# Kernel optimization log

Measured on AMD Instinct MI355X. Metric: run time of the kernel, lower is better.

The kernel has to match this reference:

```python
import jax, jax.numpy as jnp
import numpy as np

N, C, H, W = 32, 512, 56, 56
L, CT, HEAD, GROUPS = 64, 512, 16, 16
SIZE, POS_DIM = 14, 49  # PosEncoder(size=14, num_downsample=1) -> 14^2 // 4 = 49


def setup_inputs() -> dict:
    key = jax.random.key(0)
    ks = jax.random.split(key, 8)
    return {
        "feature": jax.random.normal(ks[0], (N, C, H, W), jnp.float32),
        "w_tc": jax.random.normal(ks[1], (L, C), jnp.float32) * 0.02,
        "b_tc": jnp.zeros((L,), jnp.float32),
        "w_val": jax.random.normal(ks[2], (GROUPS, CT // GROUPS, C // GROUPS), jnp.float32) * 0.02,
        "b_val": jnp.zeros((CT,), jnp.float32),
        "w_ds3": jax.random.normal(ks[3], (1, 1, 3, 3), jnp.float32) * 0.1,
        "b_ds3": jnp.zeros((1,), jnp.float32),
        "w_ds1": jax.random.normal(ks[4], (1, 1), jnp.float32) * 0.1,
        "b_ds1": jnp.zeros((1,), jnp.float32),
        "w_pos": jax.random.normal(ks[5], (POS_DIM, POS_DIM), jnp.float32) * 0.02,
        "b_pos": jnp.zeros((POS_DIM,), jnp.float32),
        "w_tok": jax.random.normal(ks[6], (CT, CT + POS_DIM), jnp.float32) * 0.02,
        "b_tok": jnp.zeros((CT,), jnp.float32),
    }


def reference(feature, w_tc, b_tc, w_val, b_val, w_ds3, b_ds3, w_ds1, b_ds1,
              w_pos, b_pos, w_tok, b_tok):
    n, c, h, w = feature.shape
    hw = h * w
    # --- static token coefficients: 1x1 conv C->L, scale, softmax over HW ---
    tc = jnp.einsum('nchw,lc->nlhw', feature, w_tc) + b_tc[None, :, None, None]
    tc = tc.reshape(n, 1, L, hw).transpose(0, 1, 3, 2) / np.sqrt(c)  # (N,1,HW,L)
    tc = jax.nn.softmax(tc, axis=2)
    # --- grouped 1x1 conv value: C -> CT (groups=16) ---
    fg = feature.reshape(n, GROUPS, c // GROUPS, hw)
    val = jnp.einsum('ngci,gdc->ngdi', fg, w_val).reshape(n, CT, hw) + b_val[None, :, None]
    val = val.reshape(n, HEAD, CT // HEAD, hw)
    # --- token aggregation: (N,h,CT/h,HW) @ (N,1,HW,L) -> (N,CT,L) ---
    tokens = jnp.matmul(val, tc).reshape(n, CT, -1)
    # --- PosEncoder: view coef maps as images, nearest-resize to 14x14 ---
    pc = tc.reshape(n * L, 1, h, w)  # torch .view memory reinterpretation
    ih = (jnp.arange(SIZE) * h) // SIZE
    iw = (jnp.arange(SIZE) * w) // SIZE
    pc = pc[:, :, ih][:, :, :, iw]  # (N*L,1,14,14) nearest interpolate
    # conv3x3 stride 2 pad 1: 14 -> 7
    pc = jax.lax.conv_general_dilated(pc, w_ds3, (2, 2), ((1, 1), (1, 1))) + b_ds3[None, :, None, None]
    # conv1x1 (1->1)
    pc = jnp.einsum('nchw,dc->ndhw', pc, w_ds1) + b_ds1[None, :, None, None]
    pc = pc.reshape(n, L, POS_DIM).transpose(0, 2, 1)  # (N,49,L)
    pos = jnp.einsum('ncl,dc->ndl', pc, w_pos) + b_pos[None, :, None]
    # --- concat + final 1x1 conv1d (CT+49 -> CT) ---
    tokens = jnp.concatenate([tokens, pos], axis=1)
    tokens = jnp.einsum('ncl,dc->ndl', tokens, w_tok) + b_tok[None, :, None]
    return tokens  # (N, CT, L)
```

## Files before the change

kernel.cpp:

```cpp
#include <hip/hip_runtime.h>
#include <cstddef>
#include <cstdint>

namespace {

constexpr int kN = 32;
constexpr int kC = 512;
constexpr int kHW = 3136;
constexpr int kL = 64;
constexpr int kCT = 512;
constexpr int kTok = 561;
constexpr int kKcat = 576;

typedef float fx4 __attribute__((ext_vector_type(4)));
typedef float f32x4 __attribute__((ext_vector_type(4)));
typedef short short8 __attribute__((ext_vector_type(8)));
typedef unsigned int u32x2 __attribute__((ext_vector_type(2)));

static __device__ inline unsigned pack_bf16(float a, float b) {
  unsigned ua = __builtin_bit_cast(unsigned, a) + 0x8000u;
  unsigned ub = __builtin_bit_cast(unsigned, b) + 0x8000u;
  return __builtin_amdgcn_perm(ub, ua, 0x07060302u);
}

__global__ __launch_bounds__(256) void build_wcat_kernel(
    const float* __restrict__ w_tok, const float* __restrict__ w_val,
    float* __restrict__ wcat) {
  int idx = blockIdx.x * 256 + threadIdx.x;
  if (idx >= kCT * kKcat) return;
  int d = idx / kKcat;
  int c = idx - d * kKcat;
  float v = 0.f;
  if (c < kCT) {
    int g = c >> 5, k = c & 31;
    const float* wt = w_tok + (size_t)d * kTok + g * 32;
    const float* wv = w_val + g * 1024 + k;
    float s = 0.f;
#pragma unroll
    for (int dp = 0; dp < 32; ++dp) s += wt[dp] * wv[dp * 32];
    v = s;
  } else if (c < kTok) {
    v = w_tok[(size_t)d * kTok + c];
  }
  wcat[idx] = v;
}

__global__ __launch_bounds__(256) void build_cst_kernel(
    const float* __restrict__ w_tok, const float* __restrict__ b_val,
    const float* __restrict__ b_tok, float* __restrict__ cst) {
  int d = blockIdx.x * 256 + threadIdx.x;
  if (d >= kCT) return;
  float s = b_tok[d];
  for (int c = 0; c < kCT; ++c) s += w_tok[(size_t)d * kTok + c] * b_val[c];
  cst[d] = s;
}

__global__ __launch_bounds__(256) void zero_pad_kernel(float* __restrict__ bcat) {
  int i = blockIdx.x * 256 + threadIdx.x;
  const int tot = kN * kL * (kKcat - kTok);
  if (i >= tot) return;
  int n = i / (kL * 15);
  int r = i - n * (kL * 15);
  int l = r / 15;
  int k = kTok + (r - l * 15);
  bcat[(size_t)n * kL * kKcat + (size_t)l * kKcat + k] = 0.f;
}

__global__ __launch_bounds__(256) void tc_gemm_kernel(
    const float* __restrict__ feat, const float* __restrict__ w_tc,
    const float* __restrict__ b_tc, float* __restrict__ tcT) {
  const int n = blockIdx.y;
  const int pb = blockIdx.x * 256;
  const int tid = threadIdx.x;
  const int wave = tid >> 6, lane = tid & 63;
  const int quad = lane >> 4, l16 = lane & 15;
  __shared__ unsigned short As[64][72];
  __shared__ unsigned short Bs[256][72];
  __shared__ float bsm[64];
  if (tid < 64) bsm[tid] = b_tc[tid];

  f32x4 acc[4][4];
#pragma unroll
  for (int i = 0; i < 4; ++i)
#pragma unroll
    for (int j = 0; j < 4; ++j) acc[i][j] = (f32x4){0.f, 0.f, 0.f, 0.f};

  const float* fb = feat + (size_t)n * kC * kHW;
  const int al = tid & 63, akg = (tid >> 6) * 16;
  const int bc4 = (tid & 15) * 4, bpl0 = (tid >> 4) * 4;

  for (int c0 = 0; c0 < kC; c0 += 64) {
    const float* asrc = w_tc + (size_t)al * kC + c0 + akg;
#pragma unroll
    for (int u = 0; u < 4; ++u) {
      fx4 v = *(const fx4*)(asrc + u * 4);
      u32x2 w = {pack_bf16(v[0], v[1]), pack_bf16(v[2], v[3])};
      *(u32x2*)&As[al][akg + u * 4] = w;
    }
#pragma unroll
    for (int pass = 0; pass < 4; ++pass) {
      int pl = bpl0 + pass * 64;
      int pe = pb + pl;
      pe = pe < 3132 ? pe : 3132;
      fx4 v0 = *(const fx4*)(fb + (size_t)(c0 + bc4 + 0) * kHW + pe);
      fx4 v1 = *(const fx4*)(fb + (size_t)(c0 + bc4 + 1) * kHW + pe);
      fx4 v2 = *(const fx4*)(fb + (size_t)(c0 + bc4 + 2) * kHW + pe);
      fx4 v3 = *(const fx4*)(fb + (size_t)(c0 + bc4 + 3) * kHW + pe);
#pragma unroll
      for (int j = 0; j < 4; ++j) {
        u32x2 w = {pack_bf16(v0[j], v1[j]), pack_bf16(v2[j], v3[j])};
        *(u32x2*)&Bs[pl + j][bc4] = w;
      }
    }
    __syncthreads();
#pragma unroll
    for (int ks = 0; ks < 2; ++ks) {
      short8 a[4], b[4];
#pragma unroll
      for (int i = 0; i < 4; ++i)
        a[i] = *(const short8*)&As[i * 16 + l16][ks * 32 + quad * 8];
#pragma unroll
      for (int j = 0; j < 4; ++j)
        b[j] = *(const short8*)&Bs[wave * 64 + j * 16 + l16][ks * 32 + quad * 8];
#pragma unroll
      for (int i = 0; i < 4; ++i)
#pragma unroll
        for (int j = 0; j < 4; ++j)
          acc[i][j] = __builtin_amdgcn_mfma_f32_16x16x32_bf16(a[i], b[j], acc[i][j], 0, 0, 0);
    }
    __syncthreads();
  }

  const float inv = 0.04419417382415922f;
  float* ob = tcT + (size_t)n * kL * kHW;
#pragma unroll
  for (int ti = 0; ti < 4; ++ti) {
#pragma unroll
    for (int tj = 0; tj < 4; ++tj) {
      int pg = pb + wave * 64 + tj * 16 + l16;
      if (pg < kHW) {
#pragma unroll
        for (int r = 0; r < 4; ++r) {
          int l = ti * 16 + quad * 4 + r;
          ob[(size_t)l * kHW + pg] = (acc[ti][tj][r] + bsm[l]) * inv;
        }
      }
    }
  }
}

__global__ __launch_bounds__(256) void softmax_stats_kernel(
    const float* __restrict__ tcT, float* __restrict__ mArr,
    float* __restrict__ invArr) {
  const int row = blockIdx.x * 4 + (threadIdx.x >> 6);
  const int lane = threadIdx.x & 63;
  const float* src = tcT + (size_t)row * kHW + lane * 4;
  fx4 x[13];
#pragma unroll
  for (int i = 0; i < 12; ++i) x[i] = *(const fx4*)(src + i * 256);
  if (lane < 16)
    x[12] = *(const fx4*)(src + 3072);
  else
    x[12] = (fx4){-1e30f, -1e30f, -1e30f, -1e30f};
  float m = -1e30f;
#pragma unroll
  for (int i = 0; i < 13; ++i)
    m = fmaxf(m, fmaxf(fmaxf(x[i][0], x[i][1]), fmaxf(x[i][2], x[i][3])));
#pragma unroll
  for (int off = 32; off >= 1; off >>= 1) m = fmaxf(m, __shfl_xor(m, off));
  float s = 0.f;
#pragma unroll
  for (int i = 0; i < 13; ++i) {
    s += __expf(x[i][0] - m) + __expf(x[i][1] - m) + __expf(x[i][2] - m) +
         __expf(x[i][3] - m);
  }
#pragma unroll
  for (int off = 32; off >= 1; off >>= 1) s += __shfl_xor(s, off);
  if (lane == 0) {
    mArr[row] = m;
    invArr[row] = 1.f / s;
  }
}

__global__ __launch_bounds__(256) void m_gemm_kernel(
    const float* __restrict__ feat, const float* __restrict__ tcT,
    const float* __restrict__ mArr, const float* __restrict__ invArr,
    float* __restrict__ part, int klen) {
  const int cb = blockIdx.x * 256;
  const int n = blockIdx.y;
  const int s = blockIdx.z;
  const int p0s = s * klen;
  const int tid = threadIdx.x;
  const int wave = tid >> 6, lane = tid & 63;
  const int quad = lane >> 4, l16 = lane & 15;
  __shared__ unsigned short As[64][72];
  __shared__ unsigned short Bs[256][72];

  const int al = tid & 63, akg = (tid >> 6) * 16;
  const float sm = mArr[n * 64 + al];
  const float si = invArr[n * 64 + al];

  f32x4 acc[4][4];
#pragma unroll
  for (int i = 0; i < 4; ++i)
#pragma unroll
    for (int j = 0; j < 4; ++j) acc[i][j] = (f32x4){0.f, 0.f, 0.f, 0.f};

  const float* tb = tcT + (size_t)(n * 64 + al) * kHW;
  const float* fb = feat + (size_t)n * kC * kHW;
  const int bkg = (tid >> 6) * 16, bcr = tid & 63;

  for (int p0 = p0s; p0 < p0s + klen; p0 += 64) {
#pragma unroll
    for (int u = 0; u < 4; ++u) {
      fx4 v = *(const fx4*)(tb + p0 + akg + u * 4);
      float e0 = __expf(v[0] - sm) * si;
      float e1 = __expf(v[1] - sm) * si;
      float e2 = __expf(v[2] - sm) * si;
      float e3 = __expf(v[3] - sm) * si;
      u32x2 w = {pack_bf16(e0, e1), pack_bf16(e2, e3)};
      *(u32x2*)&As[al][akg + u * 4] = w;
    }
#pragma unroll
    for (int pass = 0; pass < 4; ++pass) {
      int c = cb + pass * 64 + bcr;
      const float* src = fb + (size_t)c * kHW + p0 + bkg;
#pragma unroll
      for (int u = 0; u < 4; ++u) {
        fx4 v = *(const fx4*)(src + u * 4);
        u32x2 w = {pack_bf16(v[0], v[1]), pack_bf16(v[2], v[3])};
        *(u32x2*)&Bs[pass * 64 + bcr][bkg + u * 4] = w;
      }
    }
    __syncthreads();
#pragma unroll
    for (int ks = 0; ks < 2; ++ks) {
      short8 a[4], b[4];
#pragma unroll
      for (int i = 0; i < 4; ++i)
        a[i] = *(const short8*)&As[i * 16 + l16][ks * 32 + quad * 8];
#pragma unroll
      for (int j = 0; j < 4; ++j)
        b[j] = *(const short8*)&Bs[wave * 64 + j * 16 + l16][ks * 32 + quad * 8];
#pragma unroll
      for (int i = 0; i < 4; ++i)
#pragma unroll
        for (int j = 0; j < 4; ++j)
          acc[i][j] = __builtin_amdgcn_mfma_f32_16x16x32_bf16(a[i], b[j], acc[i][j], 0, 0, 0);
    }
    __syncthreads();
  }

  float* ob = part + (size_t)(s * kN + n) * kL * kCT;
#pragma unroll
  for (int ti = 0; ti < 4; ++ti) {
#pragma unroll
    for (int tj = 0; tj < 4; ++tj) {
      int cg = cb + wave * 64 + tj * 16 + l16;
#pragma unroll
      for (int r = 0; r < 4; ++r) {
        int l = ti * 16 + quad * 4 + r;
        ob[(size_t)l * kCT + cg] = acc[ti][tj][r];
      }
    }
  }
}

__global__ __launch_bounds__(256) void reduce_m_kernel(
    const float* __restrict__ part, float* __restrict__ bcat, int ksplit) {
  int i = blockIdx.x * 256 + threadIdx.x;
  if (i >= kN * kL * kCT) return;
  int n = i >> 15;
  int r = i & 32767;
  int l = r >> 9;
  int c = r & 511;
  float s = 0.f;
  for (int ss = 0; ss < ksplit; ++ss)
    s += part[(size_t)ss * kN * kL * kCT + i];
  bcat[(size_t)n * kL * kKcat + (size_t)l * kKcat + c] = s;
}

__global__ __launch_bounds__(256) void pos_conv_kernel(
    const float* __restrict__ tcT, const float* __restrict__ mArr,
    const float* __restrict__ invArr, const float* __restrict__ w3,
    const float* __restrict__ b3, const float* __restrict__ w1,
    const float* __restrict__ b1, float* __restrict__ pcl) {
  int idx = blockIdx.x * 256 + threadIdx.x;
  if (idx >= kN * kL * 49) return;
  int n = idx / (kL * 49);
  int r = idx - n * (kL * 49);
  int lp = r / 49;
  int o = r - lp * 49;
  int y = o / 7, x = o - y * 7;
  const float* tb = tcT + (size_t)n * kL * kHW;
  const float* mB = mArr + n * 64;
  const float* iB = invArr + n * 64;
  float a = 0.f;
#pragma unroll
  for (int dy = 0; dy < 3; ++dy) {
    int i = 2 * y - 1 + dy;
    if (i < 0 || i >= 14) continue;
#pragma unroll
    for (int dx = 0; dx < 3; ++dx) {
      int j = 2 * x - 1 + dx;
      if (j < 0 || j >= 14) continue;
      int t = 224 * i + 4 * j;
      int lsm = t & 63;
      int p = lp * 49 + (t >> 6);
      float raw = tb[(size_t)lsm * kHW + p];
      a += w3[dy * 3 + dx] * (__expf(raw - mB[lsm]) * iB[lsm]);
    }
  }
  pcl[idx] = (a + b3[0]) * w1[0] + b1[0];
}

__global__ __launch_bounds__(256) void pos_out_kernel(
    const float* __restrict__ pcl, const float* __restrict__ wp,
    const float* __restrict__ bp, float* __restrict__ bcat) {
  const int n = blockIdx.x;
  __shared__ float t[64 * 49];
  for (int i = threadIdx.x; i < 64 * 49; i += 256)
    t[i] = pcl[(size_t)n * 64 * 49 + i];
  __syncthreads();
  for (int o = threadIdx.x; o < 64 * 49; o += 256) {
    int l = o / 49, d = o - l * 49;
    float s = bp[d];
#pragma unroll 7
    for (int q = 0; q < 49; ++q) s += wp[d * 49 + q] * t[l * 49 + q];
    bcat[(size_t)n * kL * kKcat + (size_t)l * kKcat + kCT + d] = s;
  }
}

__global__ __launch_bounds__(256) void out_gemm_kernel(
    const float* __restrict__ wcat, const float* __restrict__ bcat,
    const float* __restrict__ cst, float* __restrict__ out) {
  const int db = blockIdx.x * 128;
  const int n = blockIdx.y;
  const int tid = threadIdx.x;
  const int wave = tid >> 6, lane = tid & 63;
  const int quad = lane >> 4, l16 = lane & 15;
  __shared__ unsigned short As[128][72];
  __shared__ unsigned short Bs[64][72];
  __shared__ float csm[128];
  if (tid < 128) csm[tid] = cst[db + tid];

  f32x4 acc[2][4];
#pragma unroll
  for (int i = 0; i < 2; ++i)
#pragma unroll
    for (int j = 0; j < 4; ++j) acc[i][j] = (f32x4){0.f, 0.f, 0.f, 0.f};

  const int ad = tid & 127, akg = (tid >> 7) * 32;
  const int bl = tid & 63, bkg = (tid >> 6) * 16;
  const float* ab = wcat + (size_t)(db + ad) * kKcat + akg;
  const float* bb = bcat + (size_t)n * kL * kKcat + (size_t)bl * kKcat + bkg;

  for (int k0 = 0; k0 < kKcat; k0 += 64) {
#pragma unroll
    for (int u = 0; u < 8; ++u) {
      fx4 v = *(const fx4*)(ab + k0 + u * 4);
      u32x2 w = {pack_bf16(v[0], v[1]), pack_bf16(v[2], v[3])};
      *(u32x2*)&As[ad][akg + u * 4] = w;
    }
#pragma unroll
    for (int u = 0; u < 4; ++u) {
      fx4 v = *(const fx4*)(bb + k0 + u * 4);
      u32x2 w = {pack_bf16(v[0], v[1]), pack_bf16(v[2], v[3])};
      *(u32x2*)&Bs[bl][bkg + u * 4] = w;
    }
    __syncthreads();
#pragma unroll
    for (int ks = 0; ks < 2; ++ks) {
      short8 a[2], b[4];
#pragma unroll
      for (int i = 0; i < 2; ++i)
        a[i] = *(const short8*)&As[wave * 32 + i * 16 + l16][ks * 32 + quad * 8];
#pragma unroll
      for (int j = 0; j < 4; ++j)
        b[j] = *(const short8*)&Bs[j * 16 + l16][ks * 32 + quad * 8];
#pragma unroll
      for (int i = 0; i < 2; ++i)
#pragma unroll
        for (int j = 0; j < 4; ++j)
          acc[i][j] = __builtin_amdgcn_mfma_f32_16x16x32_bf16(a[i], b[j], acc[i][j], 0, 0, 0);
    }
    __syncthreads();
  }

  float* ob = out + (size_t)n * kCT * kL;
#pragma unroll
  for (int ti = 0; ti < 2; ++ti) {
#pragma unroll
    for (int tj = 0; tj < 4; ++tj) {
      int lg = tj * 16 + l16;
#pragma unroll
      for (int r = 0; r < 4; ++r) {
        int dl = wave * 32 + ti * 16 + quad * 4 + r;
        ob[(size_t)(db + dl) * kL + lg] = acc[ti][tj][r] + csm[dl];
      }
    }
  }
}

}

extern "C" void kernel_launch(void* const* d_in, const int* in_sizes, int n_in,
                              void* d_out, int out_size, void* d_ws,
                              size_t ws_size, hipStream_t stream) {
  (void)in_sizes; (void)n_in; (void)out_size;
  const float* feat  = (const float*)d_in[0];
  const float* w_tc  = (const float*)d_in[1];
  const float* b_tc  = (const float*)d_in[2];
  const float* w_val = (const float*)d_in[3];
  const float* b_val = (const float*)d_in[4];
  const float* w_ds3 = (const float*)d_in[5];
  const float* b_ds3 = (const float*)d_in[6];
  const float* w_ds1 = (const float*)d_in[7];
  const float* b_ds1 = (const float*)d_in[8];
  const float* w_pos = (const float*)d_in[9];
  const float* b_pos = (const float*)d_in[10];
  const float* w_tok = (const float*)d_in[11];
  const float* b_tok = (const float*)d_in[12];
  float* out = (float*)d_out;

  float* ws = (float*)d_ws;
  size_t off = 0;
  float* tcT = ws + off;    off += (size_t)kN * kL * kHW;
  float* bcat = ws + off;   off += (size_t)kN * kL * kKcat;
  float* wcat = ws + off;   off += (size_t)kCT * kKcat;
  float* cst = ws + off;    off += kCT;
  float* mArr = ws + off;   off += kN * 64;
  float* invArr = ws + off; off += kN * 64;
  float* pcl = ws + off;    off += (size_t)kN * kL * 49;
  int ksplit = 7;
  if (ws_size < (off + (size_t)7 * kN * kL * kCT) * sizeof(float)) ksplit = 1;
  float* part = ws + off;

  build_wcat_kernel<<<(kCT * kKcat + 255) / 256, 256, 0, stream>>>(w_tok, w_val, wcat);
  build_cst_kernel<<<2, 256, 0, stream>>>(w_tok, b_val, b_tok, cst);
  zero_pad_kernel<<<(kN * kL * 15 + 255) / 256, 256, 0, stream>>>(bcat);
  tc_gemm_kernel<<<dim3(13, kN), 256, 0, stream>>>(feat, w_tc, b_tc, tcT);
  softmax_stats_kernel<<<kN * kL / 4, 256, 0, stream>>>(tcT, mArr, invArr);
  m_gemm_kernel<<<dim3(2, kN, ksplit), 256, 0, stream>>>(
      feat, tcT, mArr, invArr, part, kHW / ksplit);
  reduce_m_kernel<<<(kN * kL * kCT + 255) / 256, 256, 0, stream>>>(part, bcat, ksplit);
  pos_conv_kernel<<<(kN * kL * 49 + 255) / 256, 256, 0, stream>>>(
      tcT, mArr, invArr, w_ds3, b_ds3, w_ds1, b_ds1, pcl);
  pos_out_kernel<<<kN, 256, 0, stream>>>(pcl, w_pos, b_pos, bcat);
  out_gemm_kernel<<<dim3(4, kN), 256, 0, stream>>>(wcat, bcat, cst, out);
}
```

Before: 447.3 us.

## Fuse softmax exp into tc GEMM, store bf16 intermediates, prefetch-pipeline GEMMs

The prep kernels are merged into one launch that also converts w_tc to bf16 and zeroes the denominators. The tc GEMM now applies exp directly and writes unnormalized bf16 exponentials. It accumulates per-row sums with shared and global atomics, so the separate softmax-stats pass and the max subtraction go away. The feature GEMMs use register double-buffered global loads and read the A operand straight from global bf16. Reduce and pos-conv are fused, and the output GEMM reads bf16 operands directly without LDS staging. Skipping the max subtraction risks overflow for large logits, and bf16 intermediates reduce precision.

Result: faster. 436.1 us (-2.5%).

```diff
diff --git a/kernel.cpp b/kernel.cpp
--- a/kernel.cpp
+++ b/kernel.cpp
@@ -1,4 +1,5 @@
 #include <hip/hip_runtime.h>
+#include <hip/hip_bf16.h>
 #include <cstddef>
 #include <cstdint>
 
@@ -17,67 +18,93 @@
 typedef short short8 __attribute__((ext_vector_type(8)));
 typedef unsigned int u32x2 __attribute__((ext_vector_type(2)));
 
-static __device__ inline unsigned pack_bf16(float a, float b) {
-  unsigned ua = __builtin_bit_cast(unsigned, a) + 0x8000u;
-  unsigned ub = __builtin_bit_cast(unsigned, b) + 0x8000u;
-  return __builtin_amdgcn_perm(ub, ua, 0x07060302u);
-}
-
-__global__ __launch_bounds__(256) void build_wcat_kernel(
+static __device__ inline unsigned short bf16_1(float x) {
+  __hip_bfloat16 h = __float2bfloat16(x);
+  unsigned short u;
+  __builtin_memcpy(&u, &h, 2);
+  return u;
+}
+static __device__ inline unsigned pk2(float a, float b) {
+  __hip_bfloat162 h2 = __float22bfloat162_rn(make_float2(a, b));
+  unsigned u;
+  __builtin_memcpy(&u, &h2, 4);
+  return u;
+}
+static __device__ inline float bf2f(unsigned short h) {
+  unsigned u = (unsigned)h << 16;
+  float f;
+  __builtin_memcpy(&f, &u, 4);
+  return f;
+}
+
+__global__ __launch_bounds__(256) void prep_kernel(
     const float* __restrict__ w_tok, const float* __restrict__ w_val,
-    float* __restrict__ wcat) {
+    const float* __restrict__ b_val, const float* __restrict__ b_tok,
+    const float* __restrict__ w_tc, unsigned short* __restrict__ wcat16,
+    float* __restrict__ cst, unsigned short* __restrict__ wtc16,
+    float* __restrict__ denom, unsigned short* __restrict__ bcat16) {
   int idx = blockIdx.x * 256 + threadIdx.x;
-  if (idx >= kCT * kKcat) return;
-  int d = idx / kKcat;
-  int c = idx - d * kKcat;
-  float v = 0.f;
-  if (c < kCT) {
-    int g = c >> 5, k = c & 31;
-    const float* wt = w_tok + (size_t)d * kTok + g * 32;
-    const float* wv = w_val + g * 1024 + k;
-    float s = 0.f;
-#pragma unroll
-    for (int dp = 0; dp < 32; ++dp) s += wt[dp] * wv[dp * 32];
-    v = s;
-  } else if (c < kTok) {
-    v = w_tok[(size_t)d * kTok + c];
-  }
-  wcat[idx] = v;
-}
-
-__global__ __launch_bounds__(256) void build_cst_kernel(
-    const float* __restrict__ w_tok, const float* __restrict__ b_val,
-    const float* __restrict__ b_tok, float* __restrict__ cst) {
-  int d = blockIdx.x * 256 + threadIdx.x;
-  if (d >= kCT) return;
-  float s = b_tok[d];
-  for (int c = 0; c < kCT; ++c) s += w_tok[(size_t)d * kTok + c] * b_val[c];
-  cst[d] = s;
-}
-
-__global__ __launch_bounds__(256) void zero_pad_kernel(float* __restrict__ bcat) {
-  int i = blockIdx.x * 256 + threadIdx.x;
-  const int tot = kN * kL * (kKcat - kTok);
-  if (i >= tot) return;
-  int n = i / (kL * 15);
-  int r = i - n * (kL * 15);
-  int l = r / 15;
-  int k = kTok + (r - l * 15);
-  bcat[(size_t)n * kL * kKcat + (size_t)l * kKcat + k] = 0.f;
-}
-
-__global__ __launch_bounds__(256) void tc_gemm_kernel(
-    const float* __restrict__ feat, const float* __restrict__ w_tc,
-    const float* __restrict__ b_tc, float* __restrict__ tcT) {
+  if (idx < kCT * kKcat) {
+    int d = idx / kKcat;
+    int c = idx - d * kKcat;
+    float v = 0.f;
+    if (c < kCT) {
+      int g = c >> 5, k = c & 31;
+      const float* wt = w_tok + (size_t)d * kTok + g * 32;
+      const float* wv = w_val + g * 1024 + k;
+      float s = 0.f;
+#pragma unroll
+      for (int dp = 0; dp < 32; ++dp) s += wt[dp] * wv[dp * 32];
+      v = s;
+    } else if (c < kTok) {
+      v = w_tok[(size_t)d * kTok + c];
+    }
+    wcat16[idx] = bf16_1(v);
+    return;
+  }
+  idx -= kCT * kKcat;
+  if (idx < kCT) {
+    float s = b_tok[idx];
+    for (int c = 0; c < kCT; ++c) s += w_tok[(size_t)idx * kTok + c] * b_val[c];
+    cst[idx] = s;
+    return;
+  }
+  idx -= kCT;
+  if (idx < kL * kC) {
+    wtc16[idx] = bf16_1(w_tc[idx]);
+    return;
+  }
+  idx -= kL * kC;
+  if (idx < kN * kL) {
+    denom[idx] = 0.f;
+    return;
+  }
+  idx -= kN * kL;
+  if (idx < kN * kL * 15) {
+    int n = idx / (kL * 15);
+    int r = idx - n * (kL * 15);
+    int l = r / 15;
+    int k = kTok + (r - l * 15);
+    bcat16[(size_t)n * kL * kKcat + (size_t)l * kKcat + k] = 0;
+  }
+}
+
+__global__ __launch_bounds__(256) void tc_gemm2_kernel(
+    const float* __restrict__ feat, const unsigned short* __restrict__ wtc16,
+    const float* __restrict__ b_tc, unsigned short* __restrict__ expT,
+    float* __restrict__ denom) {
   const int n = blockIdx.y;
   const int pb = blockIdx.x * 256;
   const int tid = threadIdx.x;
   const int wave = tid >> 6, lane = tid & 63;
   const int quad = lane >> 4, l16 = lane & 15;
-  __shared__ unsigned short As[64][72];
   __shared__ unsigned short Bs[256][72];
   __shared__ float bsm[64];
-  if (tid < 64) bsm[tid] = b_tc[tid];
+  __shared__ float denom_s[64];
+  if (tid < 64) {
+    bsm[tid] = b_tc[tid];
+    denom_s[tid] = 0.f;
+  }
 
   f32x4 acc[4][4];
 #pragma unroll
@@ -86,39 +113,45 @@
     for (int j = 0; j < 4; ++j) acc[i][j] = (f32x4){0.f, 0.f, 0.f, 0.f};
 
   const float* fb = feat + (size_t)n * kC * kHW;
-  const int al = tid & 63, akg = (tid >> 6) * 16;
   const int bc4 = (tid & 15) * 4, bpl0 = (tid >> 4) * 4;
-
-  for (int c0 = 0; c0 < kC; c0 += 64) {
-    const float* asrc = w_tc + (size_t)al * kC + c0 + akg;
-#pragma unroll
-    for (int u = 0; u < 4; ++u) {
-      fx4 v = *(const fx4*)(asrc + u * 4);
-      u32x2 w = {pack_bf16(v[0], v[1]), pack_bf16(v[2], v[3])};
-      *(u32x2*)&As[al][akg + u * 4] = w;
-    }
+  int pe_[4];
+#pragma unroll
+  for (int pass = 0; pass < 4; ++pass) {
+    int pe = pb + bpl0 + pass * 64;
+    pe_[pass] = pe < 3132 ? pe : 3132;
+  }
+
+  fx4 va[4][4], vb[4][4];
+  auto LOADT = [&](int c0, fx4 (&v)[4][4]) {
 #pragma unroll
     for (int pass = 0; pass < 4; ++pass) {
-      int pl = bpl0 + pass * 64;
-      int pe = pb + pl;
-      pe = pe < 3132 ? pe : 3132;
-      fx4 v0 = *(const fx4*)(fb + (size_t)(c0 + bc4 + 0) * kHW + pe);
-      fx4 v1 = *(const fx4*)(fb + (size_t)(c0 + bc4 + 1) * kHW + pe);
-      fx4 v2 = *(const fx4*)(fb + (size_t)(c0 + bc4 + 2) * kHW + pe);
-      fx4 v3 = *(const fx4*)(fb + (size_t)(c0 + bc4 + 3) * kHW + pe);
+      const float* s = fb + (size_t)(c0 + bc4) * kHW + pe_[pass];
+#pragma unroll
+      for (int r = 0; r < 4; ++r) v[pass][r] = *(const fx4*)(s + (size_t)r * kHW);
+    }
+  };
+  auto STORET = [&](fx4 (&v)[4][4]) {
+#pragma unroll
+    for (int pass = 0; pass < 4; ++pass) {
+      int pl = bpl0 + pass * 4 * 16;
+      (void)pl;
+      int base = bpl0 + pass * 64;
 #pragma unroll
       for (int j = 0; j < 4; ++j) {
-        u32x2 w = {pack_bf16(v0[j], v1[j]), pack_bf16(v2[j], v3[j])};
-        *(u32x2*)&Bs[pl + j][bc4] = w;
+        u32x2 w = {pk2(v[pass][0][j], v[pass][1][j]),
+                   pk2(v[pass][2][j], v[pass][3][j])};
+        *(u32x2*)&Bs[base + j][bc4] = w;
       }
     }
-    __syncthreads();
+  };
+  auto COMPUTE = [&](int c0) {
 #pragma unroll
     for (int ks = 0; ks < 2; ++ks) {
       short8 a[4], b[4];
 #pragma unroll
       for (int i = 0; i < 4; ++i)
-        a[i] = *(const short8*)&As[i * 16 + l16][ks * 32 + quad * 8];
+        a[i] = *(const short8*)(wtc16 + (size_t)(i * 16 + l16) * kC + c0 +
+                                ks * 32 + quad * 8);
 #pragma unroll
       for (int j = 0; j < 4; ++j)
         b[j] = *(const short8*)&Bs[wave * 64 + j * 16 + l16][ks * 32 + quad * 8];
@@ -126,65 +159,74 @@
       for (int i = 0; i < 4; ++i)
 #pragma unroll
         for (int j = 0; j < 4; ++j)
-          acc[i][j] = __builtin_amdgcn_mfma_f32_16x16x32_bf16(a[i], b[j], acc[i][j], 0, 0, 0);
-    }
+          acc[i][j] = __builtin_amdgcn_mfma_f32_16x16x32_bf16(a[i], b[j],
+                                                              acc[i][j], 0, 0, 0);
+    }
+  };
+
+  LOADT(0, va);
+#pragma unroll
+  for (int c0 = 0; c0 < kC; c0 += 128) {
+    STORET(va);
+    __syncthreads();
+    LOADT(c0 + 64, vb);
+    COMPUTE(c0);
+    __syncthreads();
+    STORET(vb);
+    __syncthreads();
+    if (c0 + 128 < kC) LOADT(c0 + 128, va);
+    COMPUTE(c0 + 64);
     __syncthreads();
   }
 
   const float inv = 0.04419417382415922f;
-  float* ob = tcT + (size_t)n * kL * kHW;
+  unsigned short* eb = expT + (size_t)n * kL * kHW;
+  float dsum[4][4];
+#pragma unroll
+  for (int ti = 0; ti < 4; ++ti)
+#pragma unroll
+    for (int r = 0; r < 4; ++r) dsum[ti][r] = 0.f;
+
 #pragma unroll
   for (int ti = 0; ti < 4; ++ti) {
 #pragma unroll
     for (int tj = 0; tj < 4; ++tj) {
       int pg = pb + wave * 64 + tj * 16 + l16;
-      if (pg < kHW) {
-#pragma unroll
-        for (int r = 0; r < 4; ++r) {
-          int l = ti * 16 + quad * 4 + r;
-          ob[(size_t)l * kHW + pg] = (acc[ti][tj][r] + bsm[l]) * inv;
+      bool ok = pg < kHW;
+#pragma unroll
+      for (int r = 0; r < 4; ++r) {
+        int l = ti * 16 + quad * 4 + r;
+        float e = 0.f;
+        if (ok) {
+          float raw = (acc[ti][tj][r] + bsm[l]) * inv;
+          unsigned short h = bf16_1(__expf(raw));
+          eb[(size_t)l * kHW + pg] = h;
+          e = bf2f(h);
         }
+        dsum[ti][r] += e;
       }
     }
   }
-}
-
-__global__ __launch_bounds__(256) void softmax_stats_kernel(
-    const float* __restrict__ tcT, float* __restrict__ mArr,
-    float* __restrict__ invArr) {
-  const int row = blockIdx.x * 4 + (threadIdx.x >> 6);
-  const int lane = threadIdx.x & 63;
-  const float* src = tcT + (size_t)row * kHW + lane * 4;
-  fx4 x[13];
-#pragma unroll
-  for (int i = 0; i < 12; ++i) x[i] = *(const fx4*)(src + i * 256);
-  if (lane < 16)
-    x[12] = *(const fx4*)(src + 3072);
-  else
-    x[12] = (fx4){-1e30f, -1e30f, -1e30f, -1e30f};
-  float m = -1e30f;
-#pragma unroll
-  for (int i = 0; i < 13; ++i)
-    m = fmaxf(m, fmaxf(fmaxf(x[i][0], x[i][1]), fmaxf(x[i][2], x[i][3])));
-#pragma unroll
-  for (int off = 32; off >= 1; off >>= 1) m = fmaxf(m, __shfl_xor(m, off));
-  float s = 0.f;
-#pragma unroll
-  for (int i = 0; i < 13; ++i) {
-    s += __expf(x[i][0] - m) + __expf(x[i][1] - m) + __expf(x[i][2] - m) +
-         __expf(x[i][3] - m);
-  }
-#pragma unroll
-  for (int off = 32; off >= 1; off >>= 1) s += __shfl_xor(s, off);
-  if (lane == 0) {
-    mArr[row] = m;
-    invArr[row] = 1.f / s;
-  }
-}
-
-__global__ __launch_bounds__(256) void m_gemm_kernel(
-    const float* __restrict__ feat, const float* __restrict__ tcT,
-    const float* __restrict__ mArr, const float* __restrict__ invArr,
+#pragma unroll
+  for (int off = 1; off < 16; off <<= 1) {
+#pragma unroll
+    for (int ti = 0; ti < 4; ++ti)
+#pragma unroll
+      for (int r = 0; r < 4; ++r) dsum[ti][r] += __shfl_xor(dsum[ti][r], off);
+  }
+  if (l16 == 0) {
+#pragma unroll
+    for (int ti = 0; ti < 4; ++ti)
+#pragma unroll
+      for (int r = 0; r < 4; ++r)
+        atomicAdd(&denom_s[ti * 16 + quad * 4 + r], dsum[ti][r]);
+  }
+  __syncthreads();
+  if (tid < 64) atomicAdd(&denom[n * 64 + tid], denom_s[tid]);
+}
+
+__global__ __launch_bounds__(256) void m_gemm2_kernel(
+    const float* __restrict__ feat, const unsigned short* __restrict__ expT,
     float* __restrict__ part, int klen) {
   const int cb = blockIdx.x * 256;
   const int n = blockIdx.y;
@@ -193,52 +235,46 @@
   const int tid = threadIdx.x;
   const int wave = tid >> 6, lane = tid & 63;
   const int quad = lane >> 4, l16 = lane & 15;
-  __shared__ unsigned short As[64][72];
   __shared__ unsigned short Bs[256][72];
 
-  const int al = tid & 63, akg = (tid >> 6) * 16;
-  const float sm = mArr[n * 64 + al];
-  const float si = invArr[n * 64 + al];
-
   f32x4 acc[4][4];
 #pragma unroll
   for (int i = 0; i < 4; ++i)
 #pragma unroll
     for (int j = 0; j < 4; ++j) acc[i][j] = (f32x4){0.f, 0.f, 0.f, 0.f};
 
-  const float* tb = tcT + (size_t)(n * 64 + al) * kHW;
   const float* fb = feat + (size_t)n * kC * kHW;
+  const unsigned short* ebase = expT + (size_t)n * kL * kHW;
   const int bkg = (tid >> 6) * 16, bcr = tid & 63;
 
-  for (int p0 = p0s; p0 < p0s + klen; p0 += 64) {
-#pragma unroll
-    for (int u = 0; u < 4; ++u) {
-      fx4 v = *(const fx4*)(tb + p0 + akg + u * 4);
-      float e0 = __expf(v[0] - sm) * si;
-      float e1 = __expf(v[1] - sm) * si;
-      float e2 = __expf(v[2] - sm) * si;
-      float e3 = __expf(v[3] - sm) * si;
-      u32x2 w = {pack_bf16(e0, e1), pack_bf16(e2, e3)};
-      *(u32x2*)&As[al][akg + u * 4] = w;
-    }
+  fx4 va[4][4], vb[4][4];
+  auto LOADT = [&](int p0, fx4 (&v)[4][4]) {
 #pragma unroll
     for (int pass = 0; pass < 4; ++pass) {
-      int c = cb + pass * 64 + bcr;
-      const float* src = fb + (size_t)c * kHW + p0 + bkg;
+      const float* src = fb + (size_t)(cb + pass * 64 + bcr) * kHW + p0 + bkg;
+#pragma unroll
+      for (int u = 0; u < 4; ++u) v[pass][u] = *(const fx4*)(src + u * 4);
+    }
+  };
+  auto STORET = [&](fx4 (&v)[4][4]) {
+#pragma unroll
+    for (int pass = 0; pass < 4; ++pass) {
 #pragma unroll
       for (int u = 0; u < 4; ++u) {
-        fx4 v = *(const fx4*)(src + u * 4);
-        u32x2 w = {pack_bf16(v[0], v[1]), pack_bf16(v[2], v[3])};
+        u32x2 w = {pk2(v[pass][u][0], v[pass][u][1]),
+                   pk2(v[pass][u][2], v[pass][u][3])};
         *(u32x2*)&Bs[pass * 64 + bcr][bkg + u * 4] = w;
       }
     }
-    __syncthreads();
+  };
+  auto COMPUTE = [&](int p0) {
 #pragma unroll
     for (int ks = 0; ks < 2; ++ks) {
       short8 a[4], b[4];
 #pragma unroll
       for (int i = 0; i < 4; ++i)
-        a[i] = *(const short8*)&As[i * 16 + l16][ks * 32 + quad * 8];
+        a[i] = *(const short8*)(ebase + (size_t)(i * 16 + l16) * kHW + p0 +
+                                ks * 32 + quad * 8);
 #pragma unroll
       for (int j = 0; j < 4; ++j)
         b[j] = *(const short8*)&Bs[wave * 64 + j * 16 + l16][ks * 32 + quad * 8];
@@ -246,9 +282,28 @@
       for (int i = 0; i < 4; ++i)
 #pragma unroll
         for (int j = 0; j < 4; ++j)
-          acc[i][j] = __builtin_amdgcn_mfma_f32_16x16x32_bf16(a[i], b[j], acc[i][j], 0, 0, 0);
-    }
-    __syncthreads();
+          acc[i][j] = __builtin_amdgcn_mfma_f32_16x16x32_bf16(a[i], b[j],
+                                                              acc[i][j], 0, 0, 0);
+    }
+  };
+
+  const int nk = klen >> 6;
+  LOADT(p0s, va);
+  for (int t = 0; t < nk; t += 2) {
+    const int p0 = p0s + t * 64;
+    STORET(va);
+    __syncthreads();
+    const bool more1 = (t + 1) < nk;
+    if (more1) LOADT(p0 + 64, vb);
+    COMPUTE(p0);
+    __syncthreads();
+    if (more1) {
+      STORET(vb);
+      __syncthreads();
+      if (t + 2 < nk) LOADT(p0 + 128, va);
+      COMPUTE(p0 + 64);
+      __syncthreads();
+    }
   }
 
   float* ob = part + (size_t)(s * kN + n) * kL * kCT;
@@ -266,35 +321,34 @@
   }
 }
 
-__global__ __launch_bounds__(256) void reduce_m_kernel(
-    const float* __restrict__ part, float* __restrict__ bcat, int ksplit) {
-  int i = blockIdx.x * 256 + threadIdx.x;
-  if (i >= kN * kL * kCT) return;
-  int n = i >> 15;
-  int r = i & 32767;
-  int l = r >> 9;
-  int c = r & 511;
-  float s = 0.f;
-  for (int ss = 0; ss < ksplit; ++ss)
-    s += part[(size_t)ss * kN * kL * kCT + i];
-  bcat[(size_t)n * kL * kKcat + (size_t)l * kKcat + c] = s;
-}
-
-__global__ __launch_bounds__(256) void pos_conv_kernel(
-    const float* __restrict__ tcT, const float* __restrict__ mArr,
-    const float* __restrict__ invArr, const float* __restrict__ w3,
-    const float* __restrict__ b3, const float* __restrict__ w1,
-    const float* __restrict__ b1, float* __restrict__ pcl) {
+__global__ __launch_bounds__(256) void reduce_pos_kernel(
+    const float* __restrict__ part, const float* __restrict__ denom,
+    unsigned short* __restrict__ bcat16, const unsigned short* __restrict__ expT,
+    const float* __restrict__ w3, const float* __restrict__ b3,
+    const float* __restrict__ w1, const float* __restrict__ b1,
+    float* __restrict__ pcl, int ksplit) {
   int idx = blockIdx.x * 256 + threadIdx.x;
+  if (idx < kN * kL * kCT) {
+    int n = idx >> 15;
+    int r = idx & 32767;
+    int l = r >> 9;
+    int c = r & 511;
+    float s = 0.f;
+    for (int ss = 0; ss < ksplit; ++ss)
+      s += part[(size_t)ss * (kN * kL * kCT) + idx];
+    float si = 1.f / denom[n * 64 + l];
+    bcat16[(size_t)n * kL * kKcat + (size_t)l * kKcat + c] = bf16_1(s * si);
+    return;
+  }
+  idx -= kN * kL * kCT;
   if (idx >= kN * kL * 49) return;
   int n = idx / (kL * 49);
   int r = idx - n * (kL * 49);
   int lp = r / 49;
   int o = r - lp * 49;
   int y = o / 7, x = o - y * 7;
-  const float* tb = tcT + (size_t)n * kL * kHW;
-  const float* mB = mArr + n * 64;
-  const float* iB = invArr + n * 64;
+  const unsigned short* eb = expT + (size_t)n * kL * kHW;
+  const float* dB = denom + n * 64;
   float a = 0.f;
 #pragma unroll
   for (int dy = 0; dy < 3; ++dy) {
@@ -307,16 +361,16 @@
       int t = 224 * i + 4 * j;
       int lsm = t & 63;
       int p = lp * 49 + (t >> 6);
-      float raw = tb[(size_t)lsm * kHW + p];
-      a += w3[dy * 3 + dx] * (__expf(raw - mB[lsm]) * iB[lsm]);
-    }
-  }
-  pcl[idx] = (a + b3[0]) * w1[0] + b1[0];
-}
-
-__global__ __launch_bounds__(256) void pos_out_kernel(
+      float e = bf2f(eb[(size_t)lsm * kHW + p]);
+      a += w3[dy * 3 + dx] * (e / dB[lsm]);
+    }
+  }
+  pcl[(size_t)n * kL * 49 + lp * 49 + o] = (a + b3[0]) * w1[0] + b1[0];
+}
+
+__global__ __launch_bounds__(256) void pos_out2_kernel(
     const float* __restrict__ pcl, const float* __restrict__ wp,
-    const float* __restrict__ bp, float* __restrict__ bcat) {
+    const float* __restrict__ bp, unsigned short* __restrict__ bcat16) {
   const int n = blockIdx.x;
   __shared__ float t[64 * 49];
   for (int i = threadIdx.x; i < 64 * 49; i += 256)
@@ -327,77 +381,49 @@
     float s = bp[d];
 #pragma unroll 7
     for (int q = 0; q < 49; ++q) s += wp[d * 49 + q] * t[l * 49 + q];
-    bcat[(size_t)n * kL * kKcat + (size_t)l * kKcat + kCT + d] = s;
-  }
-}
-
-__global__ __launch_bounds__(256) void out_gemm_kernel(
-    const float* __restrict__ wcat, const float* __restrict__ bcat,
-    const float* __restrict__ cst, float* __restrict__ out) {
-  const int db = blockIdx.x * 128;
+    bcat16[(size_t)n * kL * kKcat + (size_t)l * kKcat + kCT + d] = bf16_1(s);
+  }
+}
+
+__global__ __launch_bounds__(256) void out_gemm2_kernel(
+    const unsigned short* __restrict__ wcat16,
+    const unsigned short* __restrict__ bcat16, const float* __restrict__ cst,
+    float* __restrict__ out) {
+  const int db = blockIdx.x * 64;
   const int n = blockIdx.y;
   const int tid = threadIdx.x;
   const int wave = tid >> 6, lane = tid & 63;
   const int quad = lane >> 4, l16 = lane & 15;
-  __shared__ unsigned short As[128][72];
-  __shared__ unsigned short Bs[64][72];
-  __shared__ float csm[128];
-  if (tid < 128) csm[tid] = cst[db + tid];
-
-  f32x4 acc[2][4];
-#pragma unroll
-  for (int i = 0; i < 2; ++i)
-#pragma unroll
-    for (int j = 0; j < 4; ++j) acc[i][j] = (f32x4){0.f, 0.f, 0.f, 0.f};
-
-  const int ad = tid & 127, akg = (tid >> 7) * 32;
-  const int bl = tid & 63, bkg = (tid >> 6) * 16;
-  const float* ab = wcat + (size_t)(db + ad) * kKcat + akg;
-  const float* bb = bcat + (size_t)n * kL * kKcat + (size_t)bl * kKcat + bkg;
-
-  for (int k0 = 0; k0 < kKcat; k0 += 64) {
-#pragma unroll
-    for (int u = 0; u < 8; ++u) {
-      fx4 v = *(const fx4*)(ab + k0 + u * 4);
-      u32x2 w = {pack_bf16(v[0], v[1]), pack_bf16(v[2], v[3])};
-      *(u32x2*)&As[ad][akg + u * 4] = w;
-    }
-#pragma unroll
-    for (int u = 0; u < 4; ++u) {
-      fx4 v = *(const fx4*)(bb + k0 + u * 4);
-      u32x2 w = {pack_bf16(v[0], v[1]), pack_bf16(v[2], v[3])};
-      *(u32x2*)&Bs[bl][bkg + u * 4] = w;
-    }
-    __syncthreads();
-#pragma unroll
-    for (int ks = 0; ks < 2; ++ks) {
-      short8 a[2], b[4];
-#pragma unroll
-      for (int i = 0; i < 2; ++i)
-        a[i] = *(const short8*)&As[wave * 32 + i * 16 + l16][ks * 32 + quad * 8];
-#pragma unroll
-      for (int j = 0; j < 4; ++j)
-        b[j] = *(const short8*)&Bs[j * 16 + l16][ks * 32 + quad * 8];
-#pragma unroll
-      for (int i = 0; i < 2; ++i)
-#pragma unroll
-        for (int j = 0; j < 4; ++j)
-          acc[i][j] = __builtin_amdgcn_mfma_f32_16x16x32_bf16(a[i], b[j], acc[i][j], 0, 0, 0);
-    }
-    __syncthreads();
+  __shared__ float csm[64];
+  if (tid < 64) csm[tid] = cst[db + tid];
+  __syncthreads();
+
+  f32x4 acc[4];
+#pragma unroll
+  for (int j = 0; j < 4; ++j) acc[j] = (f32x4){0.f, 0.f, 0.f, 0.f};
+
+  const unsigned short* ab = wcat16 + (size_t)(db + wave * 16 + l16) * kKcat;
+  const unsigned short* bb = bcat16 + (size_t)n * kL * kKcat;
+#pragma unroll
+  for (int k0 = 0; k0 < kKcat; k0 += 32) {
+    short8 a = *(const short8*)(ab + k0 + quad * 8);
+    short8 b[4];
+#pragma unroll
+    for (int j = 0; j < 4; ++j)
+      b[j] = *(const short8*)(bb + (size_t)(j * 16 + l16) * kKcat + k0 + quad * 8);
+#pragma unroll
+    for (int j = 0; j < 4; ++j)
+      acc[j] = __builtin_amdgcn_mfma_f32_16x16x32_bf16(a, b[j], acc[j], 0, 0, 0);
   }
 
   float* ob = out + (size_t)n * kCT * kL;
 #pragma unroll
-  for (int ti = 0; ti < 2; ++ti) {
-#pragma unroll
-    for (int tj = 0; tj < 4; ++tj) {
-      int lg = tj * 16 + l16;
-#pragma unroll
-      for (int r = 0; r < 4; ++r) {
-        int dl = wave * 32 + ti * 16 + quad * 4 + r;
-        ob[(size_t)(db + dl) * kL + lg] = acc[ti][tj][r] + csm[dl];
-      }
+  for (int tj = 0; tj < 4; ++tj) {
+    int lg = tj * 16 + l16;
+#pragma unroll
+    for (int r = 0; r < 4; ++r) {
+      int dl = wave * 16 + quad * 4 + r;
+      ob[(size_t)(db + dl) * kL + lg] = acc[tj][r] + csm[dl];
     }
   }
 }
@@ -425,27 +451,27 @@
 
   float* ws = (float*)d_ws;
   size_t off = 0;
-  float* tcT = ws + off;    off += (size_t)kN * kL * kHW;
-  float* bcat = ws + off;   off += (size_t)kN * kL * kKcat;
-  float* wcat = ws + off;   off += (size_t)kCT * kKcat;
-  float* cst = ws + off;    off += kCT;
-  float* mArr = ws + off;   off += kN * 64;
-  float* invArr = ws + off; off += kN * 64;
-  float* pcl = ws + off;    off += (size_t)kN * kL * 49;
+  unsigned short* expT = (unsigned short*)(ws + off);   off += (size_t)kN * kL * kHW / 2;
+  unsigned short* bcat16 = (unsigned short*)(ws + off); off += (size_t)kN * kL * kKcat / 2;
+  unsigned short* wcat16 = (unsigned short*)(ws + off); off += (size_t)kCT * kKcat / 2;
+  unsigned short* wtc16 = (unsigned short*)(ws + off);  off += (size_t)kL * kC / 2;
+  float* cst = ws + off;   off += kCT;
+  float* denom = ws + off; off += kN * kL;
+  float* pcl = ws + off;   off += (size_t)kN * kL * 49;
+  float* part = ws + off;
+
   int ksplit = 7;
   if (ws_size < (off + (size_t)7 * kN * kL * kCT) * sizeof(float)) ksplit = 1;
-  float* part = ws + off;
-
-  build_wcat_kernel<<<(kCT * kKcat + 255) / 256, 256, 0, stream>>>(w_tok, w_val, wcat);
-  build_cst_kernel<<<2, 256, 0, stream>>>(w_tok, b_val, b_tok, cst);
-  zero_pad_kernel<<<(kN * kL * 15 + 255) / 256, 256, 0, stream>>>(bcat);
-  tc_gemm_kernel<<<dim3(13, kN), 256, 0, stream>>>(feat, w_tc, b_tc, tcT);
-  softmax_stats_kernel<<<kN * kL / 4, 256, 0, stream>>>(tcT, mArr, invArr);
-  m_gemm_kernel<<<dim3(2, kN, ksplit), 256, 0, stream>>>(
-      feat, tcT, mArr, invArr, part, kHW / ksplit);
-  reduce_m_kernel<<<(kN * kL * kCT + 255) / 256, 256, 0, stream>>>(part, bcat, ksplit);
-  pos_conv_kernel<<<(kN * kL * 49 + 255) / 256, 256, 0, stream>>>(
-      tcT, mArr, invArr, w_ds3, b_ds3, w_ds1, b_ds1, pcl);
-  pos_out_kernel<<<kN, 256, 0, stream>>>(pcl, w_pos, b_pos, bcat);
-  out_gemm_kernel<<<dim3(4, kN), 256, 0, stream>>>(wcat, bcat, cst, out);
-}
+  const int klen = kHW / ksplit;
+
+  prep_kernel<<<1410, 256, 0, stream>>>(w_tok, w_val, b_val, b_tok, w_tc,
+                                        wcat16, cst, wtc16, denom, bcat16);
+  tc_gemm2_kernel<<<dim3(13, kN), 256, 0, stream>>>(feat, wtc16, b_tc, expT,
+                                                    denom);
+  m_gemm2_kernel<<<dim3(2, kN, ksplit), 256, 0, stream>>>(feat, expT, part,
+                                                          klen);
+  reduce_pos_kernel<<<4488, 256, 0, stream>>>(part, denom, bcat16, expT, w_ds3,
+                                              b_ds3, w_ds1, b_ds1, pcl, ksplit);
+  pos_out2_kernel<<<kN, 256, 0, stream>>>(pcl, w_pos, b_pos, bcat16);
+  out_gemm2_kernel<<<dim3(8, kN), 256, 0, stream>>>(wcat16, bcat16, cst, out);
+}
```
